# Kernel tuning notes

Measured on AMD Instinct MI355X. Metric: run time of the kernel, lower is better.

The kernel has to match this reference:

```python
import jax, jax.numpy as jnp
import numpy as np

N = 50000   # nodes
E = 800000  # edges (avg degree 16)
D = 96      # input feature dim
U = 96      # units (== D, so no dense_i projection)


def _glorot(key, fan_in, fan_out):
    limit = np.sqrt(6.0 / (fan_in + fan_out)).astype(np.float32)
    return jax.random.uniform(key, (fan_in, fan_out), jnp.float32, -limit, limit)


def setup_inputs() -> dict:
    key = jax.random.key(0)
    ks = jax.random.split(key, 8)
    X = jax.random.normal(ks[0], (N, D), jnp.float32)
    row = jax.random.randint(ks[1], (E,), 0, N, jnp.int32)   # destination nodes
    col = jax.random.randint(ks[2], (E,), 0, N, jnp.int32)   # source nodes
    a_vals = jax.random.uniform(ks[3], (E,), jnp.float32)    # adjacency values
    return {
        "X": X,
        "a_vals": a_vals,
        "Wn": _glorot(ks[4], D, U), "bn": jnp.zeros((U,), jnp.float32),
        "Wgi": _glorot(ks[5], D, U), "bgi": jnp.zeros((U,), jnp.float32),
        "Wgn": _glorot(ks[6], U, U), "bgn": jnp.zeros((U,), jnp.float32),
        "row": row, "col": col,
    }


def reference(X, a_vals, Wn, bn, Wgi, bgi, Wgn, bgn, row, col):
    # new_X = dense_n(X); new_X = A @ new_X  (SpMM via gather + segment_sum)
    newX = X @ Wn + bn                       # [N, U]
    msgs = a_vals[:, None] * newX[col]       # [E, U]
    agg = jax.ops.segment_sum(msgs, row, num_segments=N)  # [N, U]
    # gate = sigmoid(dense_gate_i(X) + dense_gate_n(agg))
    gate = jax.nn.sigmoid(X @ Wgi + bgi + agg @ Wgn + bgn)
    # units == inp_dim -> no dense_i; gated residual combine
    return agg * gate + X * (1.0 - gate)
```

## Files before the change

kernel.cpp:

```cpp
#include <hip/hip_runtime.h>
#include <math.h>


#define DU 96
#define DU4 24
#define NSUB 64
#define NGRP 8
#define HMAX 6656
#define CAPG_PAD 16384

typedef unsigned int uint;
typedef unsigned short ushort;
typedef __attribute__((ext_vector_type(8))) short short8;
typedef __attribute__((ext_vector_type(4))) float f32x4;

__device__ inline uint bf16r(float x) {
  uint u = __float_as_uint(x);
  return (u + 0x7FFFu + ((u >> 16) & 1u)) >> 16;
}

__global__ __launch_bounds__(256) void k_fuse1(
    const float* __restrict__ X, const float* __restrict__ Wn,
    const float* __restrict__ bn, const float* __restrict__ Wgi,
    const float* __restrict__ Wgn, const int* __restrict__ row,
    ushort* __restrict__ Xb, ushort* __restrict__ newXb,
    ushort* __restrict__ WTgi, ushort* __restrict__ WTgn,
    ushort* __restrict__ pc, int N, int E, int ntile) {
  __shared__ __align__(16) char smem[31744];
  ushort* WL = (ushort*)smem;
  typedef ushort XsRow[104];
  XsRow* Xs = (XsRow*)(smem + 18432);
  const int tid = threadIdx.x;
  const int lane = tid & 63, w = tid >> 6;
  const int m = lane & 15, q = lane >> 4;

  if ((int)blockIdx.x < ntile) {
    if (blockIdx.x == 0) {
      for (int i = tid; i < DU * DU; i += 256) {
        int n = i / DU, k = i % DU;
        WTgi[i] = (ushort)bf16r(Wgi[k * DU + n]);
      }
    } else if (blockIdx.x == 1) {
      for (int i = tid; i < DU * DU; i += 256) {
        int n = i / DU, k = i % DU;
        WTgn[i] = (ushort)bf16r(Wgn[k * DU + n]);
      }
    }
    for (int idx = tid; idx < 9216; idx += 256) {
      int j = idx & 7, ln = (idx >> 3) & 63, tk = idx >> 9;
      int ks = tk / 6, t = tk % 6;
      int k = ks * 32 + (ln >> 4) * 8 + j;
      int n = t * 16 + (ln & 15);
      WL[idx] = (ushort)bf16r(Wn[k * DU + n]);
    }
    const int row0 = blockIdx.x * 64;
    for (int i = tid; i < 64 * 48; i += 256) {
      int r = i / 48, cu = i % 48;
      int gr = row0 + r;
      uint packed = 0;
      if (gr < N) {
        float2 v = ((const float2*)X)[(size_t)gr * 48 + cu];
        packed = bf16r(v.x) | (bf16r(v.y) << 16);
        ((uint*)Xb)[(size_t)gr * 48 + cu] = packed;
      }
      *(uint*)&Xs[r][cu * 2] = packed;
    }
    __syncthreads();

    f32x4 acc[6];
#pragma unroll
    for (int t = 0; t < 6; ++t) acc[t] = (f32x4){0.f, 0.f, 0.f, 0.f};
#pragma unroll
    for (int ks = 0; ks < 3; ++ks) {
      short8 af = *(const short8*)&Xs[w * 16 + m][ks * 32 + q * 8];
#pragma unroll
      for (int t = 0; t < 6; ++t) {
        short8 bf = *(const short8*)&WL[((ks * 6 + t) * 64 + lane) * 8];
        acc[t] = __builtin_amdgcn_mfma_f32_16x16x32_bf16(af, bf, acc[t], 0, 0, 0);
      }
    }
    __syncthreads();
#pragma unroll
    for (int t = 0; t < 6; ++t) {
      int c = t * 16 + m;
      float bb = bn[c];
#pragma unroll
      for (int i = 0; i < 4; ++i)
        Xs[w * 16 + q * 4 + i][c] = (ushort)bf16r(acc[t][i] + bb);
    }
    __syncthreads();
    for (int i = tid; i < 64 * 48; i += 256) {
      int r = i / 48, cu = i % 48;
      int gr = row0 + r;
      if (gr < N) ((uint*)newXb)[(size_t)gr * 48 + cu] = *(uint*)&Xs[r][cu * 2];
    }
  } else {
    int* hist = (int*)smem;
    const int hb = (int)blockIdx.x - ntile;
    const int g = (int)(blockIdx.x & 7);
    const int sub = hb >> 3;
    const int d0 = (int)((long long)N * g >> 3);
    const int d1 = (int)((long long)N * (g + 1) >> 3);
    const int hs = d1 - d0;
    for (int j = tid; j < hs; j += 256) hist[j] = 0;
    __syncthreads();
    const int e0 = (int)(((long long)E * sub) / NSUB);
    const int e1 = (int)(((long long)E * (sub + 1)) / NSUB);
    int i = e0 + tid;
    for (; i + 1792 < e1; i += 2048) {
      int a0 = row[i], a1 = row[i + 256], a2 = row[i + 512], a3 = row[i + 768];
      int a4 = row[i + 1024], a5 = row[i + 1280], a6 = row[i + 1536], a7 = row[i + 1792];
      if (a0 >= d0 && a0 < d1) atomicAdd(&hist[a0 - d0], 1);
      if (a1 >= d0 && a1 < d1) atomicAdd(&hist[a1 - d0], 1);
      if (a2 >= d0 && a2 < d1) atomicAdd(&hist[a2 - d0], 1);
      if (a3 >= d0 && a3 < d1) atomicAdd(&hist[a3 - d0], 1);
      if (a4 >= d0 && a4 < d1) atomicAdd(&hist[a4 - d0], 1);
      if (a5 >= d0 && a5 < d1) atomicAdd(&hist[a5 - d0], 1);
      if (a6 >= d0 && a6 < d1) atomicAdd(&hist[a6 - d0], 1);
      if (a7 >= d0 && a7 < d1) atomicAdd(&hist[a7 - d0], 1);
    }
    for (; i < e1; i += 256) {
      int d = row[i];
      if (d >= d0 && d < d1) atomicAdd(&hist[d - d0], 1);
    }
    __syncthreads();
    for (int j = tid; j < hs; j += 256) pc[(size_t)sub * N + d0 + j] = (ushort)hist[j];
  }
}

__global__ __launch_bounds__(256) void k_colsum(const ushort* __restrict__ pc,
                                                ushort* __restrict__ psub,
                                                ushort* __restrict__ deg, int N) {
  int d2 = (blockIdx.x * 256 + threadIdx.x) * 2;
  if (d2 >= N) return;
  int runLo = 0, runHi = 0;
#pragma unroll 8
  for (int s = 0; s < NSUB; ++s) {
    uint v = *(const uint*)(pc + (size_t)s * N + d2);
    *(uint*)(psub + (size_t)s * N + d2) = (uint)runLo | ((uint)runHi << 16);
    runLo += (int)(v & 0xFFFFu);
    runHi += (int)(v >> 16);
  }
  *(uint*)(deg + d2) = (uint)runLo | ((uint)runHi << 16);
}

__global__ __launch_bounds__(1024) void k_off(const ushort* __restrict__ deg,
                                              int* __restrict__ off,
                                              int N, int E) {
  __shared__ int ws[16];
  const int g = blockIdx.x;
  const int tid = threadIdx.x;
  const int lane = tid & 63, wid = tid >> 6;
  const int d0 = (int)((long long)N * g >> 3);
  const int d1 = (int)((long long)N * (g + 1) >> 3);
  const int hs = d1 - d0;
  const int PT = 8;
  const int j0 = tid * PT;
  int v[PT];
  int s = 0;
#pragma unroll
  for (int k = 0; k < PT; ++k) {
    int j = j0 + k;
    v[k] = (j < hs) ? (int)deg[d0 + j] : 0;
    s += v[k];
  }
  int incl = s;
#pragma unroll
  for (int dlt = 1; dlt < 64; dlt <<= 1) {
    int t = __shfl_up(incl, dlt, 64);
    if (lane >= dlt) incl += t;
  }
  if (lane == 63) ws[wid] = incl;
  __syncthreads();
  int wexcl = 0;
#pragma unroll
  for (int k = 0; k < 16; ++k)
    if (k < wid) wexcl += ws[k];
  const int capg = (E >> 3) + CAPG_PAD;
  int running = g * capg + wexcl + (incl - s);
#pragma unroll
  for (int k = 0; k < PT; ++k) {
    int j = j0 + k;
    if (j < hs) { off[d0 + j] = running; running += v[k]; }
  }
}

__global__ __launch_bounds__(512) void k_scatter(const int* __restrict__ row,
                                                 const int* __restrict__ col,
                                                 const float* __restrict__ a_vals,
                                                 const int* __restrict__ off,
                                                 const ushort* __restrict__ psub,
                                                 int2* __restrict__ ec,
                                                 int N, int E) {
  __shared__ int cur[HMAX];
  const int g = (int)(blockIdx.x & 7);
  const int sub = (int)(blockIdx.x >> 3);
  const int d0 = (int)((long long)N * g >> 3);
  const int d1 = (int)((long long)N * (g + 1) >> 3);
  const int hs = d1 - d0;
  for (int j = threadIdx.x; j < hs; j += 512)
    cur[j] = off[d0 + j] + (int)psub[(size_t)sub * N + d0 + j];
  __syncthreads();
  const int e0 = (int)(((long long)E * sub) / NSUB);
  const int e1 = (int)(((long long)E * (sub + 1)) / NSUB);
  int i = e0 + (int)threadIdx.x;
  for (; i + 3584 < e1; i += 4096) {
    int a0 = row[i], a1 = row[i + 512], a2 = row[i + 1024], a3 = row[i + 1536];
    int a4 = row[i + 2048], a5 = row[i + 2560], a6 = row[i + 3072], a7 = row[i + 3584];
    if (a0 >= d0 && a0 < d1) {
      int s = atomicAdd(&cur[a0 - d0], 1);
      ec[s] = make_int2(col[i], __float_as_int(a_vals[i]));
    }
    if (a1 >= d0 && a1 < d1) {
      int s = atomicAdd(&cur[a1 - d0], 1);
      ec[s] = make_int2(col[i + 512], __float_as_int(a_vals[i + 512]));
    }
    if (a2 >= d0 && a2 < d1) {
      int s = atomicAdd(&cur[a2 - d0], 1);
      ec[s] = make_int2(col[i + 1024], __float_as_int(a_vals[i + 1024]));
    }
    if (a3 >= d0 && a3 < d1) {
      int s = atomicAdd(&cur[a3 - d0], 1);
      ec[s] = make_int2(col[i + 1536], __float_as_int(a_vals[i + 1536]));
    }
    if (a4 >= d0 && a4 < d1) {
      int s = atomicAdd(&cur[a4 - d0], 1);
      ec[s] = make_int2(col[i + 2048], __float_as_int(a_vals[i + 2048]));
    }
    if (a5 >= d0 && a5 < d1) {
      int s = atomicAdd(&cur[a5 - d0], 1);
      ec[s] = make_int2(col[i + 2560], __float_as_int(a_vals[i + 2560]));
    }
    if (a6 >= d0 && a6 < d1) {
      int s = atomicAdd(&cur[a6 - d0], 1);
      ec[s] = make_int2(col[i + 3072], __float_as_int(a_vals[i + 3072]));
    }
    if (a7 >= d0 && a7 < d1) {
      int s = atomicAdd(&cur[a7 - d0], 1);
      ec[s] = make_int2(col[i + 3584], __float_as_int(a_vals[i + 3584]));
    }
  }
  for (; i < e1; i += 512) {
    int d = row[i];
    if (d >= d0 && d < d1) {
      int s = atomicAdd(&cur[d - d0], 1);
      ec[s] = make_int2(col[i], __float_as_int(a_vals[i]));
    }
  }
}

__global__ __launch_bounds__(256) void k_aggGate(
    const ushort* __restrict__ Xb, const ushort* __restrict__ newXb,
    const int* __restrict__ off, const ushort* __restrict__ deg,
    const int2* __restrict__ ec, const ushort* __restrict__ WTgi,
    const ushort* __restrict__ WTgn, const float* __restrict__ bgi,
    const float* __restrict__ bgn, const float* __restrict__ X,
    float* __restrict__ Out, int N, int ntile) {
  __shared__ ushort As[64][104];
  const int tid = threadIdx.x;
  const int lane = tid & 63, w = tid >> 6;
  const int m = lane & 15, q = lane >> 4;
  const int g = (int)(blockIdx.x & 7);
  const int j = (int)(blockIdx.x >> 3);
  const int q0 = ntile >> 3, r0 = ntile & 7;
  const int sz = q0 + (g < r0 ? 1 : 0);
  if (j >= sz) return;
  const int tile = (g < r0 ? g * (q0 + 1) : r0 * (q0 + 1) + (g - r0) * q0) + j;
  const int row0 = tile * 64;

#define GCN_FMA8(ACC, V, A)                                      \
  ACC[0] = fmaf(A, __uint_as_float(V.x << 16), ACC[0]);          \
  ACC[1] = fmaf(A, __uint_as_float(V.x & 0xFFFF0000u), ACC[1]);  \
  ACC[2] = fmaf(A, __uint_as_float(V.y << 16), ACC[2]);          \
  ACC[3] = fmaf(A, __uint_as_float(V.y & 0xFFFF0000u), ACC[3]);  \
  ACC[4] = fmaf(A, __uint_as_float(V.z << 16), ACC[4]);          \
  ACC[5] = fmaf(A, __uint_as_float(V.z & 0xFFFF0000u), ACC[5]);  \
  ACC[6] = fmaf(A, __uint_as_float(V.w << 16), ACC[6]);          \
  ACC[7] = fmaf(A, __uint_as_float(V.w & 0xFFFF0000u), ACC[7])
  for (int t = tid; t < 64 * 12; t += 256) {
    const int rl = t / 12, c = t % 12;
    const int r = row0 + rl;
    float accA[8], accB[8];
#pragma unroll
    for (int k = 0; k < 8; ++k) { accA[k] = 0.f; accB[k] = 0.f; }
    if (r < N) {
      const int2* ep = ec + off[r];
      const int e1 = (int)deg[r];
      int e = 0;
      for (; e + 8 <= e1; e += 8) {
        int2 p0 = ep[e + 0];
        int2 p1 = ep[e + 1];
        int2 p2 = ep[e + 2];
        int2 p3 = ep[e + 3];
        int2 p4 = ep[e + 4];
        int2 p5 = ep[e + 5];
        int2 p6 = ep[e + 6];
        int2 p7 = ep[e + 7];
        uint4 v0 = *(const uint4*)(newXb + (size_t)p0.x * DU + c * 8);
        uint4 v1 = *(const uint4*)(newXb + (size_t)p1.x * DU + c * 8);
        uint4 v2 = *(const uint4*)(newXb + (size_t)p2.x * DU + c * 8);
        uint4 v3 = *(const uint4*)(newXb + (size_t)p3.x * DU + c * 8);
        uint4 v4 = *(const uint4*)(newXb + (size_t)p4.x * DU + c * 8);
        uint4 v5 = *(const uint4*)(newXb + (size_t)p5.x * DU + c * 8);
        uint4 v6 = *(const uint4*)(newXb + (size_t)p6.x * DU + c * 8);
        uint4 v7 = *(const uint4*)(newXb + (size_t)p7.x * DU + c * 8);
        float a0 = __int_as_float(p0.y), a1 = __int_as_float(p1.y);
        float a2 = __int_as_float(p2.y), a3 = __int_as_float(p3.y);
        float a4 = __int_as_float(p4.y), a5 = __int_as_float(p5.y);
        float a6 = __int_as_float(p6.y), a7 = __int_as_float(p7.y);
        GCN_FMA8(accA, v0, a0);
        GCN_FMA8(accB, v1, a1);
        GCN_FMA8(accA, v2, a2);
        GCN_FMA8(accB, v3, a3);
        GCN_FMA8(accA, v4, a4);
        GCN_FMA8(accB, v5, a5);
        GCN_FMA8(accA, v6, a6);
        GCN_FMA8(accB, v7, a7);
      }
      for (; e + 4 <= e1; e += 4) {
        int2 p0 = ep[e + 0];
        int2 p1 = ep[e + 1];
        int2 p2 = ep[e + 2];
        int2 p3 = ep[e + 3];
        uint4 v0 = *(const uint4*)(newXb + (size_t)p0.x * DU + c * 8);
        uint4 v1 = *(const uint4*)(newXb + (size_t)p1.x * DU + c * 8);
        uint4 v2 = *(const uint4*)(newXb + (size_t)p2.x * DU + c * 8);
        uint4 v3 = *(const uint4*)(newXb + (size_t)p3.x * DU + c * 8);
        float a0 = __int_as_float(p0.y), a1 = __int_as_float(p1.y);
        float a2 = __int_as_float(p2.y), a3 = __int_as_float(p3.y);
        GCN_FMA8(accA, v0, a0);
        GCN_FMA8(accB, v1, a1);
        GCN_FMA8(accA, v2, a2);
        GCN_FMA8(accB, v3, a3);
      }
      for (; e < e1; ++e) {
        int2 p = ep[e];
        uint4 v = *(const uint4*)(newXb + (size_t)p.x * DU + c * 8);
        float a = __int_as_float(p.y);
        GCN_FMA8(accA, v, a);
      }
    }
#pragma unroll
    for (int k = 0; k < 8; ++k) accA[k] += accB[k];
    uint4 o;
    o.x = bf16r(accA[0]) | (bf16r(accA[1]) << 16);
    o.y = bf16r(accA[2]) | (bf16r(accA[3]) << 16);
    o.z = bf16r(accA[4]) | (bf16r(accA[5]) << 16);
    o.w = bf16r(accA[6]) | (bf16r(accA[7]) << 16);
    *(uint4*)&As[rl][c * 8] = o;
  }
#undef GCN_FMA8
  __syncthreads();

  int ar = row0 + w * 16 + m;
  if (ar > N - 1) ar = N - 1;
  f32x4 acc[6];
#pragma unroll
  for (int t = 0; t < 6; ++t) acc[t] = (f32x4){0.f, 0.f, 0.f, 0.f};
#pragma unroll
  for (int ks = 0; ks < 3; ++ks) {
    short8 af = *(const short8*)(Xb + (size_t)ar * DU + ks * 32 + q * 8);
    short8 ag = *(const short8*)&As[w * 16 + m][ks * 32 + q * 8];
#pragma unroll
    for (int t = 0; t < 6; ++t) {
      short8 bf = *(const short8*)(WTgi + (size_t)(t * 16 + m) * DU + ks * 32 + q * 8);
      acc[t] = __builtin_amdgcn_mfma_f32_16x16x32_bf16(af, bf, acc[t], 0, 0, 0);
      short8 bg = *(const short8*)(WTgn + (size_t)(t * 16 + m) * DU + ks * 32 + q * 8);
      acc[t] = __builtin_amdgcn_mfma_f32_16x16x32_bf16(ag, bg, acc[t], 0, 0, 0);
    }
  }

#pragma unroll
  for (int t = 0; t < 6; ++t) {
    const int c = t * 16 + m;
    const float bb = bgi[c] + bgn[c];
#pragma unroll
    for (int i = 0; i < 4; ++i) {
      const int rl = w * 16 + q * 4 + i;
      const int gr = row0 + rl;
      if (gr < N) {
        float z = acc[t][i] + bb;
        float gate = 1.f / (1.f + __expf(-z));
        float xv = X[(size_t)gr * DU + c];
        float av = __uint_as_float((uint)As[rl][c] << 16);
        Out[(size_t)gr * DU + c] = xv + gate * (av - xv);
      }
    }
  }
}

extern "C" void kernel_launch(void* const* d_in, const int* in_sizes, int n_in,
                              void* d_out, int out_size, void* d_ws, size_t ws_size,
                              hipStream_t stream) {
  const float* X      = (const float*)d_in[0];
  const float* a_vals = (const float*)d_in[1];
  const float* Wn     = (const float*)d_in[2];
  const float* bn     = (const float*)d_in[3];
  const float* Wgi    = (const float*)d_in[4];
  const float* bgi    = (const float*)d_in[5];
  const float* Wgn    = (const float*)d_in[6];
  const float* bgn    = (const float*)d_in[7];
  const int*   row    = (const int*)d_in[8];
  const int*   col    = (const int*)d_in[9];
  float* out = (float*)d_out;

  const int N = in_sizes[0] / DU;
  const int E = in_sizes[1];
  const int ntile = (N + 63) / 64;
  const int G1 = ntile + NSUB * NGRP;
  const int capg = (E >> 3) + CAPG_PAD;

  int2*   ec    = (int2*)d_ws;
  ushort* Xb    = (ushort*)(ec + (size_t)NGRP * capg);
  ushort* newXb = Xb + (size_t)N * DU;
  ushort* WTgi  = newXb + (size_t)N * DU;
  ushort* WTgn  = WTgi + DU * DU;
  int*    off   = (int*)(WTgn + DU * DU);
  ushort* deg   = (ushort*)(off + ((N + 3) & ~3));
  ushort* pc    = deg + (((size_t)N + 7) & ~7ull);
  ushort* psub  = pc + (size_t)NSUB * N;

  k_fuse1  <<<G1, 256, 0, stream>>>(X, Wn, bn, Wgi, Wgn, row,
                                    Xb, newXb, WTgi, WTgn, pc, N, E, ntile);
  k_colsum <<<(N / 2 + 255) / 256, 256, 0, stream>>>(pc, psub, deg, N);
  k_off    <<<NGRP, 1024, 0, stream>>>(deg, off, N, E);
  k_scatter<<<NSUB * NGRP, 512, 0, stream>>>(row, col, a_vals, off, psub, ec, N, E);
  k_aggGate<<<((ntile + 7) / 8) * 8, 256, 0, stream>>>(Xb, newXb, off, deg, ec,
                                                       WTgi, WTgn, bgi, bgn,
                                                       X, out, N, ntile);
}
```

Baseline: 200.8 us.

## Use 512-thread blocks in aggGate, split MFMA columns, and vectorize gated epilogue via LDS

Doubles the aggGate block to 512 threads, so each row tile's gather work is spread over more threads and each wave computes only half of the gate output columns. Gate values are staged in a new shared-memory array, and the final combine is rewritten as coalesced float4 reads of X and float4 writes of Out. The grouped tile-to-block mapping is replaced with a plain blockIdx mapping. This adds shared memory and an extra barrier, and the launch bound of 6 may put pressure on registers.

```diff
diff --git a/kernel.cpp b/kernel.cpp
--- a/kernel.cpp
+++ b/kernel.cpp
@@ -249,24 +249,19 @@
   }
 }
 
-__global__ __launch_bounds__(256) void k_aggGate(
+__global__ __launch_bounds__(512, 6) void k_aggGate(
     const ushort* __restrict__ Xb, const ushort* __restrict__ newXb,
     const int* __restrict__ off, const ushort* __restrict__ deg,
     const int2* __restrict__ ec, const ushort* __restrict__ WTgi,
     const ushort* __restrict__ WTgn, const float* __restrict__ bgi,
     const float* __restrict__ bgn, const float* __restrict__ X,
-    float* __restrict__ Out, int N, int ntile) {
+    float* __restrict__ Out, int N) {
   __shared__ ushort As[64][104];
+  __shared__ float Gs[64][100];
   const int tid = threadIdx.x;
   const int lane = tid & 63, w = tid >> 6;
   const int m = lane & 15, q = lane >> 4;
-  const int g = (int)(blockIdx.x & 7);
-  const int j = (int)(blockIdx.x >> 3);
-  const int q0 = ntile >> 3, r0 = ntile & 7;
-  const int sz = q0 + (g < r0 ? 1 : 0);
-  if (j >= sz) return;
-  const int tile = (g < r0 ? g * (q0 + 1) : r0 * (q0 + 1) + (g - r0) * q0) + j;
-  const int row0 = tile * 64;
+  const int row0 = (int)blockIdx.x * 64;
 
 #define GCN_FMA8(ACC, V, A)                                      \
   ACC[0] = fmaf(A, __uint_as_float(V.x << 16), ACC[0]);          \
@@ -277,7 +272,7 @@
   ACC[5] = fmaf(A, __uint_as_float(V.z & 0xFFFF0000u), ACC[5]);  \
   ACC[6] = fmaf(A, __uint_as_float(V.w << 16), ACC[6]);          \
   ACC[7] = fmaf(A, __uint_as_float(V.w & 0xFFFF0000u), ACC[7])
-  for (int t = tid; t < 64 * 12; t += 256) {
+  for (int t = tid; t < 64 * 12; t += 512) {
     const int rl = t / 12, c = t % 12;
     const int r = row0 + rl;
     float accA[8], accB[8];
@@ -352,39 +347,54 @@
 #undef GCN_FMA8
   __syncthreads();
 
-  int ar = row0 + w * 16 + m;
+  const int rq = w >> 1, th = w & 1;
+  int ar = row0 + rq * 16 + m;
   if (ar > N - 1) ar = N - 1;
-  f32x4 acc[6];
-#pragma unroll
-  for (int t = 0; t < 6; ++t) acc[t] = (f32x4){0.f, 0.f, 0.f, 0.f};
+  f32x4 acc[3];
+#pragma unroll
+  for (int t = 0; t < 3; ++t) acc[t] = (f32x4){0.f, 0.f, 0.f, 0.f};
 #pragma unroll
   for (int ks = 0; ks < 3; ++ks) {
     short8 af = *(const short8*)(Xb + (size_t)ar * DU + ks * 32 + q * 8);
-    short8 ag = *(const short8*)&As[w * 16 + m][ks * 32 + q * 8];
-#pragma unroll
-    for (int t = 0; t < 6; ++t) {
-      short8 bf = *(const short8*)(WTgi + (size_t)(t * 16 + m) * DU + ks * 32 + q * 8);
+    short8 ag = *(const short8*)&As[rq * 16 + m][ks * 32 + q * 8];
+#pragma unroll
+    for (int t = 0; t < 3; ++t) {
+      const int ct = th * 3 + t;
+      short8 bf = *(const short8*)(WTgi + (size_t)(ct * 16 + m) * DU + ks * 32 + q * 8);
       acc[t] = __builtin_amdgcn_mfma_f32_16x16x32_bf16(af, bf, acc[t], 0, 0, 0);
-      short8 bg = *(const short8*)(WTgn + (size_t)(t * 16 + m) * DU + ks * 32 + q * 8);
+      short8 bg = *(const short8*)(WTgn + (size_t)(ct * 16 + m) * DU + ks * 32 + q * 8);
       acc[t] = __builtin_amdgcn_mfma_f32_16x16x32_bf16(ag, bg, acc[t], 0, 0, 0);
     }
   }
-
-#pragma unroll
-  for (int t = 0; t < 6; ++t) {
-    const int c = t * 16 + m;
+#pragma unroll
+  for (int t = 0; t < 3; ++t) {
+    const int c = (th * 3 + t) * 16 + m;
     const float bb = bgi[c] + bgn[c];
 #pragma unroll
     for (int i = 0; i < 4; ++i) {
-      const int rl = w * 16 + q * 4 + i;
-      const int gr = row0 + rl;
-      if (gr < N) {
-        float z = acc[t][i] + bb;
-        float gate = 1.f / (1.f + __expf(-z));
-        float xv = X[(size_t)gr * DU + c];
-        float av = __uint_as_float((uint)As[rl][c] << 16);
-        Out[(size_t)gr * DU + c] = xv + gate * (av - xv);
-      }
+      float z = acc[t][i] + bb;
+      Gs[rq * 16 + q * 4 + i][c] = 1.f / (1.f + __expf(-z));
+    }
+  }
+  __syncthreads();
+
+  for (int j = tid; j < 64 * DU4; j += 512) {
+    int r = j / DU4, c = j % DU4;
+    int gr = row0 + r;
+    if (gr < N) {
+      float4 xv = ((const float4*)X)[(size_t)gr * DU4 + c];
+      uint2 av = *(const uint2*)&As[r][c * 4];
+      float a0 = __uint_as_float(av.x << 16);
+      float a1 = __uint_as_float(av.x & 0xFFFF0000u);
+      float a2 = __uint_as_float(av.y << 16);
+      float a3 = __uint_as_float(av.y & 0xFFFF0000u);
+      const float* gp = &Gs[r][c * 4];
+      float4 o;
+      o.x = xv.x + gp[0] * (a0 - xv.x);
+      o.y = xv.y + gp[1] * (a1 - xv.y);
+      o.z = xv.z + gp[2] * (a2 - xv.z);
+      o.w = xv.w + gp[3] * (a3 - xv.w);
+      ((float4*)Out)[(size_t)gr * DU4 + c] = o;
     }
   }
 }
@@ -425,7 +435,6 @@
   k_colsum <<<(N / 2 + 255) / 256, 256, 0, stream>>>(pc, psub, deg, N);
   k_off    <<<NGRP, 1024, 0, stream>>>(deg, off, N, E);
   k_scatter<<<NSUB * NGRP, 512, 0, stream>>>(row, col, a_vals, off, psub, ec, N, E);
-  k_aggGate<<<((ntile + 7) / 8) * 8, 256, 0, stream>>>(Xb, newXb, off, deg, ec,
-                                                       WTgi, WTgn, bgi, bgn,
-                                                       X, out, N, ntile);
-}
+  k_aggGate<<<ntile, 512, 0, stream>>>(Xb, newXb, off, deg, ec, WTgi, WTgn,
+                                       bgi, bgn, X, out, N);
+}
```

After: 211.9 us. 5.5% more time.
